# Kernel tuning notes

Hardware: AMD Instinct MI355X
Metric: run time of the kernel (lower is better)

The kernel has to match this reference:

```python
import jax, jax.numpy as jnp
import numpy as np
from jax import lax

N = 50000
IN_C = 64
OUT_C = 128
RATIO = 1.0 / 6.0
K = 8
EPS = 1e-5
BIG = 1e10  # sentinel instead of inf (bf16-safe)


def fps_indices(pos, m):
    """Deterministic farthest-point sampling (start at index 0), single graph."""
    n = pos.shape[0]

    def step(carry, _):
        min_d, last = carry
        d = jnp.sum((pos - pos[last]) ** 2, axis=-1)  # [N]
        min_d = jnp.minimum(min_d, d)
        nxt = jnp.argmax(min_d).astype(jnp.int32)
        return (min_d, nxt), nxt

    init = (jnp.full((n,), BIG, pos.dtype), jnp.array(0, jnp.int32))
    _, rest = lax.scan(step, init, None, length=m - 1)
    return jnp.concatenate([jnp.zeros((1,), jnp.int32), rest])


def knn_indices(pos, sub_pos, k):
    """For each of M query centers, indices of k nearest source points. [M,k]"""
    # squared distances: ||y||^2 - 2 y.x + ||x||^2  -> [M, N]
    d = (jnp.sum(sub_pos ** 2, -1, keepdims=True)
         - 2.0 * sub_pos @ pos.T
         + jnp.sum(pos ** 2, -1)[None, :])
    _, col = lax.top_k(-d, k)  # k smallest distances
    return col


def graph_norm(h, weight, bias, mean_scale):
    # single graph: statistics over all nodes (dim 0)
    mean = jnp.mean(h, axis=0, keepdims=True)
    centered = h - mean_scale * mean
    var = jnp.mean(centered ** 2, axis=0, keepdims=True)
    return centered * lax.rsqrt(var + EPS) * weight + bias


def setup_inputs() -> dict:
    key = jax.random.key(0)
    k1, k2, k3 = jax.random.split(key, 3)
    return {
        "x": jax.random.normal(k1, (N, IN_C), jnp.float32),
        "pos": jax.random.normal(k2, (N, 3), jnp.float32),
        "batch": jnp.zeros((N,), jnp.int64),
        "lin_w": jax.random.normal(k3, (OUT_C, IN_C), jnp.float32) * (1.0 / np.sqrt(IN_C)),
        "lin_b": jnp.zeros((OUT_C,), jnp.float32),
        "gn_weight": jnp.ones((OUT_C,), jnp.float32),
        "gn_bias": jnp.zeros((OUT_C,), jnp.float32),
        "gn_mean_scale": jnp.ones((OUT_C,), jnp.float32),
    }


def reference(x, pos, batch, lin_w, lin_b, gn_weight, gn_bias, gn_mean_scale):
    m = int(np.ceil(N * RATIO))
    id_clusters = fps_indices(pos, m)                 # [M]
    sub_batch = batch[id_clusters]                    # [M]
    sub_pos = pos[id_clusters]                        # [M,3]
    col = knn_indices(pos, sub_pos, K)                # [M,K] neighbor source ids
    # MLP: Linear -> GraphNorm -> ReLU (plain_last=False)
    h = x @ lin_w.T + lin_b                           # [N,OUT_C]
    h = jax.nn.relu(graph_norm(h, gn_weight, gn_bias, gn_mean_scale))
    # scatter_max over exactly K neighbors per cluster == max over K axis
    out = jnp.max(h[col], axis=1)                     # [M,OUT_C]
    return out, sub_pos, sub_batch
```

## Files before the change

kernel.cpp:

```cpp
#include <hip/hip_runtime.h>
#include <stdint.h>

typedef unsigned long long u64;
typedef uint32_t u32;

#define NPTS 50000
#define MCL  8334
#define NITER 8333
#define INC 64
#define OUTC 128
#define FPS_G 49
#define FPS_T 1024
#define KCH 8
#define CPTS 6250
#define KTILE 250
#define NTILE 25
#define QBLK 33
#define RB 782

#define WS_SLOTS 0u
#define WS_IDS   1024u
#define WS_POSF4 34816u
#define WS_CAND  834816u
#define WS_COL   5101824u
#define WS_PSUM  5368512u
#define WS_PSQ   5768896u
#define WS_AB    6169280u
#define WS_TOTAL 6170304u

#define OUT_POS   (MCL * OUTC)
#define OUT_BATCH (OUT_POS + MCL * 3)

__global__ void k_prep(const float* __restrict__ pos, float4* __restrict__ posf4,
                       u64* __restrict__ slots) {
    int i = blockIdx.x * blockDim.x + threadIdx.x;
    if (blockIdx.x == 0 && threadIdx.x < 128) slots[threadIdx.x] = 0ull;
    if (i < NPTS) {
        float x = pos[3 * i], y = pos[3 * i + 1], z = pos[3 * i + 2];
        float pp = __fadd_rn(__fadd_rn(__fmul_rn(x, x), __fmul_rn(y, y)), __fmul_rn(z, z));
        posf4[i] = make_float4(x, y, z, pp);
    }
}

__global__ void __launch_bounds__(FPS_T) k_fps(const float4* __restrict__ posf4,
                                               u64* __restrict__ slots,
                                               int* __restrict__ ids) {
    const int tid = threadIdx.x, bid = blockIdx.x;
    const int g = bid * FPS_T + tid;
    const bool act = g < NPTS;
    float px = 0.f, py = 0.f, pz = 0.f;
    if (act) { float4 p = posf4[g]; px = p.x; py = p.y; pz = p.z; }
    float md = act ? 1e10f : 0.0f;
    const u32 inv16 = act ? (0xFFFFu - (u32)g) : 0u;
    const int lane = tid & 63, wid = tid >> 6;
    __shared__ u64 wred[16];
    __shared__ u64 swin;
    int cur = 0;
    if (bid == 0 && tid == 0) ids[0] = 0;
    for (int it = 0; it < NITER; ++it) {
        const u64 tag = (u64)(it + 1);
        const int row = (it & 1) << 6;
        float4 w = posf4[cur];
        float dx = __fsub_rn(px, w.x), dy = __fsub_rn(py, w.y), dz = __fsub_rn(pz, w.z);
        float d = __fadd_rn(__fadd_rn(__fmul_rn(dx, dx), __fmul_rn(dy, dy)), __fmul_rn(dz, dz));
        md = fminf(md, d);
        u64 key = ((u64)__float_as_uint(md) << 32) | ((u64)inv16 << 16) | tag;
        #pragma unroll
        for (int o = 32; o >= 1; o >>= 1) {
            u64 other = __shfl_xor(key, o);
            if (other > key) key = other;
        }
        if (lane == 0) wred[wid] = key;
        __syncthreads();
        if (wid == 0) {
            u64 k2 = (lane < 16) ? wred[lane] : 0ull;
            #pragma unroll
            for (int o = 8; o >= 1; o >>= 1) {
                u64 other = __shfl_xor(k2, o);
                if (other > k2) k2 = other;
            }
            if (lane == 0)
                __hip_atomic_store(&slots[row + bid], k2, __ATOMIC_RELEASE, __HIP_MEMORY_SCOPE_AGENT);
            u64 v = 0ull;
            if (lane < FPS_G) {
                const u64* sp = &slots[row + lane];
                do {
                    v = __hip_atomic_load(sp, __ATOMIC_ACQUIRE, __HIP_MEMORY_SCOPE_AGENT);
                } while ((v & 0xFFFFull) != tag);
            }
            #pragma unroll
            for (int o = 32; o >= 1; o >>= 1) {
                u64 other = __shfl_xor(v, o);
                if (other > v) v = other;
            }
            if (lane == 0) swin = v;
        }
        __syncthreads();
        cur = 0xFFFF - (int)((swin >> 16) & 0xFFFFull);
        if (bid == 0 && tid == 0) ids[it + 1] = cur;
    }
}

__global__ void k_subs(const float* __restrict__ pos, const int* __restrict__ batch,
                       const int* __restrict__ ids, float* __restrict__ out) {
    int m = blockIdx.x * blockDim.x + threadIdx.x;
    if (m < MCL) {
        int id = ids[m];
        out[OUT_POS + m * 3 + 0] = pos[id * 3 + 0];
        out[OUT_POS + m * 3 + 1] = pos[id * 3 + 1];
        out[OUT_POS + m * 3 + 2] = pos[id * 3 + 2];
        out[OUT_BATCH + m] = (float)batch[id];
    }
}

__device__ __forceinline__ u32 f2sort(float d) {
    u32 u = __float_as_uint(d);
    return (u & 0x80000000u) ? ~u : (u | 0x80000000u);
}

__global__ void __launch_bounds__(256) k_knn(const float4* __restrict__ posf4,
                                             const int* __restrict__ ids,
                                             u64* __restrict__ cand) {
    __shared__ float4 tile[KTILE];
    const int bid = blockIdx.x, tid = threadIdx.x;
    const int qb = bid % QBLK, chunk = bid / QBLK;
    const int q = qb * 256 + tid;
    const bool act = q < MCL;
    float qx = 0.f, qy = 0.f, qz = 0.f, qq = 0.f;
    if (act) { float4 p = posf4[ids[q]]; qx = p.x; qy = p.y; qz = p.z; qq = p.w; }
    u64 r[8];
    #pragma unroll
    for (int j = 0; j < 8; ++j) r[j] = ~0ull;
    const int base0 = chunk * CPTS;
    for (int t = 0; t < NTILE; ++t) {
        __syncthreads();
        if (tid < KTILE) tile[tid] = posf4[base0 + t * KTILE + tid];
        __syncthreads();
        if (act) {
            for (int p = 0; p < KTILE; ++p) {
                float4 f = tile[p];
                float c = __fmul_rn(qx, f.x);
                c = fmaf(qy, f.y, c);
                c = fmaf(qz, f.z, c);
                float d = __fadd_rn(__fsub_rn(qq, __fmul_rn(2.0f, c)), f.w);
                u64 key = ((u64)f2sort(d) << 32) | (u32)(base0 + t * KTILE + p);
                if (key < r[7]) {
                    r[7] = key;
                    #pragma unroll
                    for (int jj = 7; jj >= 1; --jj) {
                        if (r[jj] < r[jj - 1]) { u64 tk = r[jj]; r[jj] = r[jj - 1]; r[jj - 1] = tk; }
                    }
                }
            }
        }
    }
    if (act) {
        #pragma unroll
        for (int j = 0; j < 8; ++j) cand[(size_t)q * 64 + chunk * 8 + j] = r[j];
    }
}

__global__ void k_merge(const u64* __restrict__ cand, int* __restrict__ col) {
    int q = blockIdx.x * blockDim.x + threadIdx.x;
    if (q >= MCL) return;
    u64 r[8];
    #pragma unroll
    for (int j = 0; j < 8; ++j) r[j] = ~0ull;
    for (int k = 0; k < 64; ++k) {
        u64 key = cand[(size_t)q * 64 + k];
        if (key < r[7]) {
            r[7] = key;
            #pragma unroll
            for (int jj = 7; jj >= 1; --jj) {
                if (r[jj] < r[jj - 1]) { u64 tk = r[jj]; r[jj] = r[jj - 1]; r[jj - 1] = tk; }
            }
        }
    }
    #pragma unroll
    for (int j = 0; j < 8; ++j) col[q * 8 + j] = (int)(r[j] & 0xFFFFFFFFull);
}

__global__ void __launch_bounds__(256) k_linstats(const float* __restrict__ x,
                                                  const float* __restrict__ w,
                                                  const float* __restrict__ b,
                                                  float* __restrict__ psum,
                                                  float* __restrict__ psq) {
    __shared__ float xs[64 * 65];
    __shared__ float ws[128 * 65];
    const int bid = blockIdx.x, tid = threadIdx.x;
    const int row0 = bid * 64;
    for (int idx = tid; idx < 64 * 64; idx += 256) {
        int r = idx >> 6, j = idx & 63;
        int gr = row0 + r;
        xs[r * 65 + j] = (gr < NPTS) ? x[gr * 64 + j] : 0.0f;
    }
    for (int idx = tid; idx < 128 * 64; idx += 256) {
        int c = idx >> 6, j = idx & 63;
        ws[c * 65 + j] = w[idx];
    }
    __syncthreads();
    const int ch = tid & 127, grp = tid >> 7;
    const float lb = b[ch];
    float s = 0.f, sq = 0.f;
    for (int rr = 0; rr < 32; ++rr) {
        int r = grp * 32 + rr;
        float acc = lb;
        #pragma unroll 8
        for (int j = 0; j < 64; ++j) acc = fmaf(xs[r * 65 + j], ws[ch * 65 + j], acc);
        if (row0 + r < NPTS) { s += acc; sq = fmaf(acc, acc, sq); }
    }
    __syncthreads();
    float* red = xs;
    red[grp * 128 + ch] = s;
    red[256 + grp * 128 + ch] = sq;
    __syncthreads();
    if (grp == 0) {
        psum[bid * 128 + ch] = red[ch] + red[128 + ch];
        psq[bid * 128 + ch] = red[256 + ch] + red[256 + 128 + ch];
    }
}

__global__ void k_finalize(const float* __restrict__ psum, const float* __restrict__ psq,
                           const float* __restrict__ gnw, const float* __restrict__ gnb,
                           const float* __restrict__ gms, float* __restrict__ ab) {
    int ch = threadIdx.x;
    float s = 0.f, q = 0.f;
    for (int bk = 0; bk < RB; ++bk) { s += psum[bk * 128 + ch]; q += psq[bk * 128 + ch]; }
    float m = s / (float)NPTS;
    float e2 = q / (float)NPTS;
    float msc = gms[ch];
    float mm = msc * m;
    float var = e2 - 2.0f * mm * m + mm * mm;
    float inv = rsqrtf(var + 1e-5f);
    float a = inv * gnw[ch];
    ab[ch] = a;
    ab[128 + ch] = gnb[ch] - mm * a;
}

__global__ void __launch_bounds__(128) k_gather(const float* __restrict__ x,
                                                const float* __restrict__ w,
                                                const float* __restrict__ b,
                                                const int* __restrict__ col,
                                                const float* __restrict__ ab,
                                                float* __restrict__ out) {
    __shared__ float xs[8 * 64];
    __shared__ float ws[128 * 65];
    __shared__ int cl[8];
    const int m = blockIdx.x, tid = threadIdx.x;
    if (tid < 8) cl[tid] = col[m * 8 + tid];
    __syncthreads();
    for (int idx = tid; idx < 512; idx += 128) {
        int r = idx >> 6, j = idx & 63;
        xs[idx] = x[cl[r] * 64 + j];
    }
    for (int idx = tid; idx < 128 * 64; idx += 128) {
        int c = idx >> 6, j = idx & 63;
        ws[c * 65 + j] = w[idx];
    }
    __syncthreads();
    const int ch = tid;
    const float lb = b[ch];
    float hmax = -3.402823466e38f, hmin = 3.402823466e38f;
    #pragma unroll
    for (int r = 0; r < 8; ++r) {
        float acc = lb;
        #pragma unroll 8
        for (int j = 0; j < 64; ++j) acc = fmaf(xs[r * 64 + j], ws[ch * 65 + j], acc);
        hmax = fmaxf(hmax, acc);
        hmin = fminf(hmin, acc);
    }
    float a = ab[ch], be = ab[128 + ch];
    float v = (a >= 0.0f) ? hmax : hmin;
    out[m * OUTC + ch] = fmaxf(0.0f, fmaf(a, v, be));
}

extern "C" void kernel_launch(void* const* d_in, const int* in_sizes, int n_in,
                              void* d_out, int out_size, void* d_ws, size_t ws_size,
                              hipStream_t stream) {
    const float* x     = (const float*)d_in[0];
    const float* pos   = (const float*)d_in[1];
    const int*   batch = (const int*)d_in[2];
    const float* lin_w = (const float*)d_in[3];
    const float* lin_b = (const float*)d_in[4];
    const float* gnw   = (const float*)d_in[5];
    const float* gnb   = (const float*)d_in[6];
    const float* gms   = (const float*)d_in[7];
    float* out = (float*)d_out;

    if (ws_size < (size_t)WS_TOTAL) return;

    char* ws = (char*)d_ws;
    u64*    slots = (u64*)(ws + WS_SLOTS);
    int*    ids   = (int*)(ws + WS_IDS);
    float4* posf4 = (float4*)(ws + WS_POSF4);
    u64*    cand  = (u64*)(ws + WS_CAND);
    int*    col   = (int*)(ws + WS_COL);
    float*  psum  = (float*)(ws + WS_PSUM);
    float*  psq   = (float*)(ws + WS_PSQ);
    float*  ab    = (float*)(ws + WS_AB);

    k_prep<<<196, 256, 0, stream>>>(pos, posf4, slots);
    k_fps<<<FPS_G, FPS_T, 0, stream>>>(posf4, slots, ids);
    k_subs<<<QBLK, 256, 0, stream>>>(pos, batch, ids, out);
    k_knn<<<QBLK * KCH, 256, 0, stream>>>(posf4, ids, cand);
    k_merge<<<QBLK, 256, 0, stream>>>(cand, col);
    k_linstats<<<RB, 256, 0, stream>>>(x, lin_w, lin_b, psum, psq);
    k_finalize<<<1, 128, 0, stream>>>(psum, psq, gnw, gnb, gms, ab);
    k_gather<<<MCL, 128, 0, stream>>>(x, lin_w, lin_b, col, ab, out);
}
```

Measured before the change: 33.60 ms.

## Replace multi-block FPS with single-block spatially sorted FPS using bounding-box pruning

Farthest-point sampling moves from 49 cooperating blocks that synchronise through global atomic slots on every iteration to a single 1024-thread block. Points are first Morton-sorted into a 16^3 grid so each thread owns 49 spatially coherent points. A per-thread bounding-box lower bound lets a thread skip its distance updates when the new center cannot lower its current max. This removes the cross-block global synchronisation per iteration, at the cost of serial per-thread work and two extra single-block preprocessing kernels. The kNN chunk count is also halved (4 chunks of 12500 points), which shrinks the candidate merge.

```diff
diff --git a/kernel.cpp b/kernel.cpp
--- a/kernel.cpp
+++ b/kernel.cpp
@@ -7,34 +7,32 @@
 #define NPTS 50000
 #define MCL  8334
 #define NITER 8333
-#define INC 64
 #define OUTC 128
-#define FPS_G 49
-#define FPS_T 1024
-#define KCH 8
-#define CPTS 6250
+#define PTT  49
+#define KCH 4
+#define CPTS 12500
 #define KTILE 250
-#define NTILE 25
+#define NTILE 50
 #define QBLK 33
 #define RB 782
-
-#define WS_SLOTS 0u
-#define WS_IDS   1024u
-#define WS_POSF4 34816u
-#define WS_CAND  834816u
-#define WS_COL   5101824u
-#define WS_PSUM  5368512u
-#define WS_PSQ   5768896u
-#define WS_AB    6169280u
-#define WS_TOTAL 6170304u
+#define NCELL 4096
+
+#define WS_IDS   0u
+#define WS_BBOX  33792u
+#define WS_POSF4 33824u
+#define WS_SPOS  833824u
+#define WS_CAND  1636640u
+#define WS_COL   3770144u
+#define WS_PSUM  4036832u
+#define WS_PSQ   4437216u
+#define WS_AB    4837600u
+#define WS_TOTAL 4838624u
 
 #define OUT_POS   (MCL * OUTC)
 #define OUT_BATCH (OUT_POS + MCL * 3)
 
-__global__ void k_prep(const float* __restrict__ pos, float4* __restrict__ posf4,
-                       u64* __restrict__ slots) {
+__global__ void k_prep(const float* __restrict__ pos, float4* __restrict__ posf4) {
     int i = blockIdx.x * blockDim.x + threadIdx.x;
-    if (blockIdx.x == 0 && threadIdx.x < 128) slots[threadIdx.x] = 0ull;
     if (i < NPTS) {
         float x = pos[3 * i], y = pos[3 * i + 1], z = pos[3 * i + 2];
         float pp = __fadd_rn(__fadd_rn(__fmul_rn(x, x), __fmul_rn(y, y)), __fmul_rn(z, z));
@@ -42,62 +40,162 @@
     }
 }
 
-__global__ void __launch_bounds__(FPS_T) k_fps(const float4* __restrict__ posf4,
-                                               u64* __restrict__ slots,
+__global__ void __launch_bounds__(1024) k_bbox(const float* __restrict__ pos,
+                                               float* __restrict__ bbox) {
+    __shared__ float red[16][6];
+    const int tid = threadIdx.x, lane = tid & 63, wid = tid >> 6;
+    float mnx = 3.4e38f, mny = 3.4e38f, mnz = 3.4e38f;
+    float mxx = -3.4e38f, mxy = -3.4e38f, mxz = -3.4e38f;
+    for (int i = tid; i < NPTS; i += 1024) {
+        float x = pos[3 * i], y = pos[3 * i + 1], z = pos[3 * i + 2];
+        mnx = fminf(mnx, x); mxx = fmaxf(mxx, x);
+        mny = fminf(mny, y); mxy = fmaxf(mxy, y);
+        mnz = fminf(mnz, z); mxz = fmaxf(mxz, z);
+    }
+    #pragma unroll
+    for (int o = 32; o >= 1; o >>= 1) {
+        mnx = fminf(mnx, __shfl_xor(mnx, o)); mxx = fmaxf(mxx, __shfl_xor(mxx, o));
+        mny = fminf(mny, __shfl_xor(mny, o)); mxy = fmaxf(mxy, __shfl_xor(mxy, o));
+        mnz = fminf(mnz, __shfl_xor(mnz, o)); mxz = fmaxf(mxz, __shfl_xor(mxz, o));
+    }
+    if (lane == 0) {
+        red[wid][0] = mnx; red[wid][1] = mny; red[wid][2] = mnz;
+        red[wid][3] = mxx; red[wid][4] = mxy; red[wid][5] = mxz;
+    }
+    __syncthreads();
+    if (tid == 0) {
+        for (int w2 = 1; w2 < 16; ++w2) {
+            red[0][0] = fminf(red[0][0], red[w2][0]);
+            red[0][1] = fminf(red[0][1], red[w2][1]);
+            red[0][2] = fminf(red[0][2], red[w2][2]);
+            red[0][3] = fmaxf(red[0][3], red[w2][3]);
+            red[0][4] = fmaxf(red[0][4], red[w2][4]);
+            red[0][5] = fmaxf(red[0][5], red[w2][5]);
+        }
+        bbox[0] = red[0][0]; bbox[1] = red[0][1]; bbox[2] = red[0][2];
+        bbox[3] = 16.0f / (fmaxf(red[0][3] - red[0][0], 1e-20f) * 1.000001f);
+        bbox[4] = 16.0f / (fmaxf(red[0][4] - red[0][1], 1e-20f) * 1.000001f);
+        bbox[5] = 16.0f / (fmaxf(red[0][5] - red[0][2], 1e-20f) * 1.000001f);
+    }
+}
+
+__device__ __forceinline__ u32 mort(int cx, int cy, int cz) {
+    u32 m = 0;
+    #pragma unroll
+    for (int b = 0; b < 4; ++b)
+        m |= (((cx >> b) & 1) << (3 * b)) | (((cy >> b) & 1) << (3 * b + 1)) |
+             (((cz >> b) & 1) << (3 * b + 2));
+    return m;
+}
+
+__device__ __forceinline__ u32 cell_of(float x, float y, float z, const float* bb) {
+    int cx = (int)((x - bb[0]) * bb[3]);
+    int cy = (int)((y - bb[1]) * bb[4]);
+    int cz = (int)((z - bb[2]) * bb[5]);
+    cx = min(15, max(0, cx)); cy = min(15, max(0, cy)); cz = min(15, max(0, cz));
+    return mort(cx, cy, cz);
+}
+
+__global__ void __launch_bounds__(1024) k_sort(const float* __restrict__ pos,
+                                               const float* __restrict__ bbox,
+                                               float4* __restrict__ spos) {
+    __shared__ u32 hist[NCELL];
+    __shared__ u32 wsum[16];
+    const int tid = threadIdx.x, lane = tid & 63, wid = tid >> 6;
+    float bb[6];
+    #pragma unroll
+    for (int j = 0; j < 6; ++j) bb[j] = bbox[j];
+    for (int i = tid; i < NCELL; i += 1024) hist[i] = 0u;
+    __syncthreads();
+    for (int i = tid; i < NPTS; i += 1024) {
+        float x = pos[3 * i], y = pos[3 * i + 1], z = pos[3 * i + 2];
+        atomicAdd(&hist[cell_of(x, y, z, bb)], 1u);
+    }
+    __syncthreads();
+    u32 h0 = hist[tid * 4], h1 = hist[tid * 4 + 1], h2 = hist[tid * 4 + 2], h3 = hist[tid * 4 + 3];
+    u32 ts = h0 + h1 + h2 + h3;
+    u32 sc = ts;
+    #pragma unroll
+    for (int o = 1; o < 64; o <<= 1) { u32 n = __shfl_up(sc, o); if (lane >= o) sc += n; }
+    if (lane == 63) wsum[wid] = sc;
+    __syncthreads();
+    u32 woff = 0;
+    for (int w2 = 0; w2 < wid; ++w2) woff += wsum[w2];
+    u32 excl = woff + sc - ts;
+    hist[tid * 4 + 0] = excl;
+    hist[tid * 4 + 1] = excl + h0;
+    hist[tid * 4 + 2] = excl + h0 + h1;
+    hist[tid * 4 + 3] = excl + h0 + h1 + h2;
+    __syncthreads();
+    for (int i = tid; i < NPTS; i += 1024) {
+        float x = pos[3 * i], y = pos[3 * i + 1], z = pos[3 * i + 2];
+        u32 dst = atomicAdd(&hist[cell_of(x, y, z, bb)], 1u);
+        spos[dst] = make_float4(x, y, z, __uint_as_float((u32)i));
+    }
+}
+
+__global__ void __launch_bounds__(1024) k_fps2(const float4* __restrict__ spos,
+                                               const float4* __restrict__ posf4,
+                                               const float* __restrict__ pos,
                                                int* __restrict__ ids) {
-    const int tid = threadIdx.x, bid = blockIdx.x;
-    const int g = bid * FPS_T + tid;
-    const bool act = g < NPTS;
-    float px = 0.f, py = 0.f, pz = 0.f;
-    if (act) { float4 p = posf4[g]; px = p.x; py = p.y; pz = p.z; }
-    float md = act ? 1e10f : 0.0f;
-    const u32 inv16 = act ? (0xFFFFu - (u32)g) : 0u;
-    const int lane = tid & 63, wid = tid >> 6;
-    __shared__ u64 wred[16];
-    __shared__ u64 swin;
-    int cur = 0;
-    if (bid == 0 && tid == 0) ids[0] = 0;
+    const int tid = threadIdx.x, lane = tid & 63, wid = tid >> 6;
+    const int base = tid * PTT;
+    __shared__ u64 wred[2][16];
+    float md[PTT];
+    int nv = NPTS - base; nv = nv < 0 ? 0 : (nv > PTT ? PTT : nv);
+    float bxn = 3.4e38f, byn = 3.4e38f, bzn = 3.4e38f;
+    float bxm = -3.4e38f, bym = -3.4e38f, bzm = -3.4e38f;
+    #pragma unroll
+    for (int i = 0; i < PTT; ++i) {
+        md[i] = 1e10f;
+        if (i < nv) {
+            float4 s = spos[base + i];
+            bxn = fminf(bxn, s.x); bxm = fmaxf(bxm, s.x);
+            byn = fminf(byn, s.y); bym = fmaxf(bym, s.y);
+            bzn = fminf(bzn, s.z); bzm = fmaxf(bzm, s.z);
+        }
+    }
+    u64 tkey = 0ull;
+    float tmax = 1e10f;
+    float cx = pos[0], cy = pos[1], cz = pos[2];
+    if (tid == 0) ids[0] = 0;
     for (int it = 0; it < NITER; ++it) {
-        const u64 tag = (u64)(it + 1);
-        const int row = (it & 1) << 6;
-        float4 w = posf4[cur];
-        float dx = __fsub_rn(px, w.x), dy = __fsub_rn(py, w.y), dz = __fsub_rn(pz, w.z);
-        float d = __fadd_rn(__fadd_rn(__fmul_rn(dx, dx), __fmul_rn(dy, dy)), __fmul_rn(dz, dz));
-        md = fminf(md, d);
-        u64 key = ((u64)__float_as_uint(md) << 32) | ((u64)inv16 << 16) | tag;
+        float ddx = fmaxf(0.0f, fmaxf(bxn - cx, cx - bxm));
+        float ddy = fmaxf(0.0f, fmaxf(byn - cy, cy - bym));
+        float ddz = fmaxf(0.0f, fmaxf(bzn - cz, cz - bzm));
+        float lb = (ddx * ddx + ddy * ddy + ddz * ddz) * 0.999999f;
+        if (nv > 0 && lb < tmax) {
+            u64 nk = 0ull;
+            #pragma unroll
+            for (int i = 0; i < PTT; ++i) {
+                if (i < nv) {
+                    float4 s = spos[base + i];
+                    float dx = __fsub_rn(s.x, cx), dy = __fsub_rn(s.y, cy), dz = __fsub_rn(s.z, cz);
+                    float d = __fadd_rn(__fadd_rn(__fmul_rn(dx, dx), __fmul_rn(dy, dy)),
+                                        __fmul_rn(dz, dz));
+                    float m = fminf(md[i], d);
+                    md[i] = m;
+                    u64 k = ((u64)__float_as_uint(m) << 32) |
+                            (u64)(0xFFFFu - (u32)__float_as_uint(s.w));
+                    if (k > nk) nk = k;
+                }
+            }
+            tkey = nk;
+            tmax = __uint_as_float((u32)(nk >> 32));
+        }
+        u64 k = tkey;
         #pragma unroll
-        for (int o = 32; o >= 1; o >>= 1) {
-            u64 other = __shfl_xor(key, o);
-            if (other > key) key = other;
-        }
-        if (lane == 0) wred[wid] = key;
+        for (int o = 32; o >= 1; o >>= 1) { u64 ot = __shfl_xor(k, o); if (ot > k) k = ot; }
+        if (lane == 0) wred[it & 1][wid] = k;
         __syncthreads();
-        if (wid == 0) {
-            u64 k2 = (lane < 16) ? wred[lane] : 0ull;
-            #pragma unroll
-            for (int o = 8; o >= 1; o >>= 1) {
-                u64 other = __shfl_xor(k2, o);
-                if (other > k2) k2 = other;
-            }
-            if (lane == 0)
-                __hip_atomic_store(&slots[row + bid], k2, __ATOMIC_RELEASE, __HIP_MEMORY_SCOPE_AGENT);
-            u64 v = 0ull;
-            if (lane < FPS_G) {
-                const u64* sp = &slots[row + lane];
-                do {
-                    v = __hip_atomic_load(sp, __ATOMIC_ACQUIRE, __HIP_MEMORY_SCOPE_AGENT);
-                } while ((v & 0xFFFFull) != tag);
-            }
-            #pragma unroll
-            for (int o = 32; o >= 1; o >>= 1) {
-                u64 other = __shfl_xor(v, o);
-                if (other > v) v = other;
-            }
-            if (lane == 0) swin = v;
-        }
-        __syncthreads();
-        cur = 0xFFFF - (int)((swin >> 16) & 0xFFFFull);
-        if (bid == 0 && tid == 0) ids[it + 1] = cur;
+        u64 v = (lane < 16) ? wred[it & 1][lane] : 0ull;
+        #pragma unroll
+        for (int o = 8; o >= 1; o >>= 1) { u64 ot = __shfl_xor(v, o); if (ot > v) v = ot; }
+        v = __shfl(v, 0);
+        int orig = 0xFFFF - (int)(v & 0xFFFFull);
+        if (tid == 0) ids[it + 1] = orig;
+        float4 c = posf4[orig];
+        cx = c.x; cy = c.y; cz = c.z;
     }
 }
 
@@ -156,7 +254,7 @@
     }
     if (act) {
         #pragma unroll
-        for (int j = 0; j < 8; ++j) cand[(size_t)q * 64 + chunk * 8 + j] = r[j];
+        for (int j = 0; j < 8; ++j) cand[(size_t)q * 32 + chunk * 8 + j] = r[j];
     }
 }
 
@@ -166,8 +264,8 @@
     u64 r[8];
     #pragma unroll
     for (int j = 0; j < 8; ++j) r[j] = ~0ull;
-    for (int k = 0; k < 64; ++k) {
-        u64 key = cand[(size_t)q * 64 + k];
+    for (int k = 0; k < 32; ++k) {
+        u64 key = cand[(size_t)q * 32 + k];
         if (key < r[7]) {
             r[7] = key;
             #pragma unroll
@@ -290,17 +388,20 @@
     if (ws_size < (size_t)WS_TOTAL) return;
 
     char* ws = (char*)d_ws;
-    u64*    slots = (u64*)(ws + WS_SLOTS);
     int*    ids   = (int*)(ws + WS_IDS);
+    float*  bbox  = (float*)(ws + WS_BBOX);
     float4* posf4 = (float4*)(ws + WS_POSF4);
+    float4* spos  = (float4*)(ws + WS_SPOS);
     u64*    cand  = (u64*)(ws + WS_CAND);
     int*    col   = (int*)(ws + WS_COL);
     float*  psum  = (float*)(ws + WS_PSUM);
     float*  psq   = (float*)(ws + WS_PSQ);
     float*  ab    = (float*)(ws + WS_AB);
 
-    k_prep<<<196, 256, 0, stream>>>(pos, posf4, slots);
-    k_fps<<<FPS_G, FPS_T, 0, stream>>>(posf4, slots, ids);
+    k_prep<<<196, 256, 0, stream>>>(pos, posf4);
+    k_bbox<<<1, 1024, 0, stream>>>(pos, bbox);
+    k_sort<<<1, 1024, 0, stream>>>(pos, bbox, spos);
+    k_fps2<<<1, 1024, 0, stream>>>(spos, posf4, pos, ids);
     k_subs<<<QBLK, 256, 0, stream>>>(pos, batch, ids, out);
     k_knn<<<QBLK * KCH, 256, 0, stream>>>(posf4, ids, cand);
     k_merge<<<QBLK, 256, 0, stream>>>(cand, col);
```

New measurement: 64.89 ms. +93.1%, slower.
